# Optimization experiments

Measured on AMD Instinct MI355X. Metric: run time of the kernel, lower is better.

The kernel has to match this reference:

```python
import jax, jax.numpy as jnp
import numpy as np

NY, NX = 2048, 2048
DX = 5.0
DT = 0.8
BETA = 4.0
RHO = 1.0 / 9.81
EPS_ETA = 0.001
MANNING2 = 0.055 ** 2
PAD = ((0, 0), (0, 0), (1, 1), (1, 1))


def _conv3(x, w):
    # 1-channel 3x3 stencil, VALID padding: [1,1,H+2,W+2] -> [1,1,H,W]
    return jax.lax.conv_general_dilated(
        x, w, window_strides=(1, 1), padding='VALID',
        dimension_numbers=('NCHW', 'OIHW', 'NCHW'))


def _bc_u(u):
    # zero left/right columns, copy top/bottom rows (free-slip in y, no-flow in x)
    p = jnp.pad(u, PAD)
    p = p.at[:, :, 0, :].set(p[:, :, 1, :])
    p = p.at[:, :, -1, :].set(p[:, :, -2, :])
    return p


def _bc_v(v):
    # copy left/right columns, zero top/bottom rows
    p = jnp.pad(v, PAD)
    p = p.at[:, :, :, 0].set(p[:, :, :, 1])
    p = p.at[:, :, :, -1].set(p[:, :, :, -2])
    return p


def _bc_eta(h):
    # Neumann (copy) on all four sides; column copies first, then rows (matches torch order)
    p = jnp.pad(h, PAD)
    p = p.at[:, :, :, -1].set(p[:, :, :, -2])
    p = p.at[:, :, :, 0].set(p[:, :, :, 1])
    p = p.at[:, :, -1, :].set(p[:, :, -2, :])
    p = p.at[:, :, 0, :].set(p[:, :, 1, :])
    return p


def _k_pg(wpad, u, v, w1, w2, w3):
    # Petrov-Galerkin dissipation coefficient
    amp = 0.5 * (jnp.abs(u) + jnp.abs(v)) / DX  # = 1/2 dx^-2 (|u|dx + |v|dx)
    num = 0.25 * DX * jnp.abs(amp * _conv3(wpad, w1))
    den = EPS_ETA + 0.5 * (jnp.abs(_conv3(wpad, w2)) + jnp.abs(_conv3(wpad, w3))) / DX ** 2
    return num / den


def _pg_vector(uu, vv, u, v, k3, w1, w2, w3):
    k_u = _k_pg(uu, u, v, w1, w2, w3)
    k_v = _k_pg(vv, u, v, w1, w2, w3)
    k_uu = jnp.pad(jnp.minimum(k_u, k3), PAD)
    k_vv = jnp.pad(jnp.minimum(k_v, k3), PAD)
    k_x = 0.5 * (k_u * _conv3(uu, w1) + _conv3(uu * k_uu, w1) - u * _conv3(k_uu, w1))
    k_y = 0.5 * (k_v * _conv3(vv, w1) + _conv3(vv * k_vv, w1) - v * _conv3(k_vv, w1))
    return k_x, k_y


def _pg_scalar(hh, h, u, v, k3, w1, w2, w3):
    k_u = _k_pg(hh, u, v, w1, w2, w3)
    k_uu = jnp.pad(jnp.minimum(k_u, k3), PAD)
    return 0.5 * (k_u * _conv3(hh, w1) + _conv3(hh * k_uu, w1) - h * _conv3(k_uu, w1))


def _forward(values_u, values_v, values_H, values_h, k1, k2, k3,
             source_h, dif_values_h, values_hh, w1, w2, w3, wm):
    diag = -w1[0, 0, 1, 1]
    uu = _bc_u(values_u)
    vv = _bc_v(values_v)
    k_x, k_y = _pg_vector(uu, vv, values_u, values_v, k3, w1, w2, w3)
    hp = _bc_eta(values_h)
    # predictor (half) step
    b_u = (k_x * DT - values_u * _conv3(uu, w2) * DT - values_v * _conv3(uu, w3) * DT) * 0.5 + values_u
    b_v = (k_y * DT - values_u * _conv3(vv, w2) * DT - values_v * _conv3(vv, w3) * DT) * 0.5 + values_v
    b_u = b_u - _conv3(hp, w2) * DT
    b_v = b_v - _conv3(hp, w3) * DT
    b_uu = _bc_u(b_u)  # note: padded fields built BEFORE friction division, as in source
    b_vv = _bc_v(b_v)
    depth43 = jnp.maximum(k1, values_H + values_h) ** (4.0 / 3.0)
    sigma_q = jnp.sqrt(b_u ** 2 + b_v ** 2) * MANNING2 / depth43
    b_u = b_u / (1.0 + sigma_q * DT / RHO)
    b_v = b_v / (1.0 + sigma_q * DT / RHO)
    # corrector (full) step
    k_x, k_y = _pg_vector(b_uu, b_vv, b_u, b_v, k3, w1, w2, w3)
    u_n = values_u + k_x * DT - b_u * _conv3(b_uu, w2) * DT - b_v * _conv3(b_uu, w3) * DT
    v_n = values_v + k_y * DT - b_u * _conv3(b_vv, w2) * DT - b_v * _conv3(b_vv, w3) * DT
    u_n = u_n - _conv3(hp, w2) * DT
    v_n = v_n - _conv3(hp, w3) * DT
    sigma_q = jnp.sqrt(u_n ** 2 + v_n ** 2) * MANNING2 / depth43
    u_n = u_n / (1.0 + sigma_q * DT / RHO)
    v_n = v_n / (1.0 + sigma_q * DT / RHO)
    uu = _bc_u(u_n)
    vv = _bc_v(v_n)
    eta1 = jnp.maximum(k2, values_H + values_h)
    eta2 = jnp.maximum(k1, values_H + values_h)
    e1p = _bc_eta(eta1)
    b = BETA * RHO * (
        -_conv3(e1p, w2) * u_n - _conv3(e1p, w3) * v_n
        - eta1 * _conv3(uu, w2) - eta1 * _conv3(vv, w3)
        + _pg_scalar(e1p, eta1, u_n, v_n, k3, w1, w2, w3)
        - _conv3(_bc_eta(dif_values_h), wm) / DT
        + source_h) / (DT * eta2)
    # two Jacobi iterations for the wave (pressure) equation
    coef = BETA * RHO / (DT ** 2 * eta2)
    denom = diag + coef
    hh = values_hh
    for _ in range(2):
        hh = hh - (-_conv3(_bc_eta(hh), w1) + coef * hh) / denom + b / denom
    h_new = values_h + hh
    dif_h = h_new - values_h
    hhp = _bc_eta(hh)
    u_n = u_n - _conv3(hhp, w2) * DT / RHO
    v_n = v_n - _conv3(hhp, w3) * DT / RHO
    return (u_n, v_n, h_new, hh, b, dif_h)


def setup_inputs() -> dict:
    key = jax.random.key(0)
    k = jax.random.split(key, 6)
    shape = (1, 1, NY, NX)
    w1 = jnp.asarray(np.array([[1, 1, 1], [1, -8, 1], [1, 1, 1]], np.float32) / 3.0 / DX ** 2).reshape(1, 1, 3, 3)
    w2 = jnp.asarray(np.array([[-1, 0, 1], [-4, 0, 4], [-1, 0, 1]], np.float32) / 12.0 / DX).reshape(1, 1, 3, 3)
    w3 = jnp.transpose(w2, (0, 1, 3, 2))
    wm = jnp.asarray(np.array([[1, 4, 1], [4, 16, 4], [1, 4, 1]], np.float32) / 36.0).reshape(1, 1, 3, 3)
    return {
        'values_u': jax.random.normal(k[0], shape, jnp.float32) * 0.5,
        'values_v': jax.random.normal(k[1], shape, jnp.float32) * 0.5,
        'values_H': jax.random.uniform(k[2], shape, jnp.float32) * 10.0,  # bathymetric depth
        'values_h': jax.random.normal(k[3], shape, jnp.float32) * 0.1,   # free-surface elevation
        'k1': jnp.full(shape, EPS_ETA, jnp.float32),
        'k2': jnp.zeros(shape, jnp.float32),
        'k3': jnp.full(shape, DX ** 2 * 0.1 / DT, jnp.float32),
        'source_h': jax.random.normal(k[4], shape, jnp.float32) * 0.01,
        'dif_values_h': jax.random.normal(k[5], shape, jnp.float32) * 0.01,
        'values_hh': jnp.zeros(shape, jnp.float32),
        'w1': w1, 'w2': w2, 'w3': w3, 'wm': wm,
    }


def reference(values_u, values_v, values_H, values_h, k1, k2, k3,
              source_h, dif_values_h, values_hh, w1, w2, w3, wm):
    return _forward(values_u, values_v, values_H, values_h, k1, k2, k3,
                    source_h, dif_values_h, values_hh, w1, w2, w3, wm)
```

## Files before the change

kernel.cpp:

```cpp
#include <hip/hip_runtime.h>
#include <math.h>


#define NY 2048
#define NX 2048
#define BX 64
#define BY 8
#define GX (NX / BX)
#define GY (NY / BY)
#define KH (BY + 2)
#define KW (BX + 2)
#define TH (BY + 4)
#define TW (BX + 4)

#define DXf   5.0f
#define DTf   0.8f
#define EPSf  0.001f
#define K3f   3.125f

__device__ constexpr float M2f    = (float)(0.055 * 0.055);
__device__ constexpr float RHO_   = (float)(1.0 / 9.81);
__device__ constexpr float BRf    = (float)(4.0 / 9.81);
__device__ constexpr float DT2f   = (float)(0.8 * 0.8);
__device__ constexpr float C43f   = (float)(4.0 / 3.0);
__device__ constexpr float DTRHO  = 0.8f / RHO_;
__device__ constexpr float INVDT  = 1.0f / 0.8f;
__device__ constexpr float CBRDT2 = BRf / DT2f;

#define W1E ((1.0f / 3.0f) / 25.0f)
#define W1C ((-8.0f / 3.0f) / 25.0f)
#define DIAGf ((8.0f / 3.0f) / 25.0f)
#define W2A ((1.0f / 12.0f) / 5.0f)
#define W2B ((4.0f / 12.0f) / 5.0f)
#define WMA (1.0f / 36.0f)
#define WMB (4.0f / 36.0f)
#define WMC (16.0f / 36.0f)

__device__ __forceinline__ int iclamp(int v, int lo, int hi) {
    return v < lo ? lo : (v > hi ? hi : v);
}

__device__ __forceinline__ float frcp(float x) {
    float r = __builtin_amdgcn_rcpf(x);
    return r * (2.0f - x * r);
}

struct N9 { float m[9]; };

template<bool SAFE, int BC>
__device__ __forceinline__ float ld(const float* __restrict__ p, int y, int x) {
    if constexpr (SAFE) {
        if constexpr (BC == 0) {
            if ((unsigned)x >= (unsigned)NX) return 0.0f;
            y = iclamp(y, 0, NY - 1);
        } else if constexpr (BC == 1) {
            if ((unsigned)y >= (unsigned)NY) return 0.0f;
            x = iclamp(x, 0, NX - 1);
        } else {
            y = iclamp(y, 0, NY - 1);
            x = iclamp(x, 0, NX - 1);
        }
    }
    return p[y * NX + x];
}

template<bool SAFE, int BC>
__device__ __forceinline__ N9 ld9(const float* __restrict__ p, int y, int x) {
    N9 n;
#pragma unroll
    for (int dy = 0; dy < 3; ++dy)
#pragma unroll
        for (int dx = 0; dx < 3; ++dx)
            n.m[dy * 3 + dx] = ld<SAFE, BC>(p, y + dy - 1, x + dx - 1);
    return n;
}

template<int W>
__device__ __forceinline__ N9 lds9(const float a[][W], int r, int c) {
    N9 n;
#pragma unroll
    for (int dy = 0; dy < 3; ++dy)
#pragma unroll
        for (int dx = 0; dx < 3; ++dx)
            n.m[dy * 3 + dx] = a[r + dy][c + dx];
    return n;
}

__device__ __forceinline__ float conv1(const N9& n) {
    float nb = n.m[0] + n.m[1] + n.m[2] + n.m[3] + n.m[5] + n.m[6] + n.m[7] + n.m[8];
    return W1E * nb + W1C * n.m[4];
}
__device__ __forceinline__ float conv2(const N9& n) {
    return W2A * ((n.m[2] - n.m[0]) + (n.m[8] - n.m[6])) + W2B * (n.m[5] - n.m[3]);
}
__device__ __forceinline__ float conv3(const N9& n) {
    return W2A * ((n.m[6] - n.m[0]) + (n.m[8] - n.m[2])) + W2B * (n.m[7] - n.m[1]);
}

__device__ __forceinline__ float kpgf(float uq, float vq, float c1, float c2, float c3) {
    float amp = 0.5f * (fabsf(uq) + fabsf(vq)) * 0.2f;
    float num = 1.25f * fabsf(amp * c1);
    float den = EPSf + 0.5f * (fabsf(c2) + fabsf(c3)) * 0.04f;
    return num * frcp(den);
}

__device__ __forceinline__ void prodk(const N9& f, const N9& k, float& pw, float& kw) {
    float nbk = k.m[0] + k.m[1] + k.m[2] + k.m[3] + k.m[5] + k.m[6] + k.m[7] + k.m[8];
    float nbp = f.m[0] * k.m[0] + f.m[1] * k.m[1] + f.m[2] * k.m[2] + f.m[3] * k.m[3]
              + f.m[5] * k.m[5] + f.m[6] * k.m[6] + f.m[7] * k.m[7] + f.m[8] * k.m[8];
    kw = W1E * nbk + W1C * k.m[4];
    pw = W1E * nbp + W1C * (f.m[4] * k.m[4]);
}

template<bool SAFE>
__device__ __forceinline__ void kA_body(
    const float* __restrict__ u, const float* __restrict__ v,
    const float* __restrict__ H, const float* __restrict__ h,
    float* __restrict__ bupre, float* __restrict__ bvpre,
    float* __restrict__ buo, float* __restrict__ bvo,
    float (*skum)[KW], float (*skvm)[KW])
{
    const int tx0 = blockIdx.x * BX, ty0 = blockIdx.y * BY;
    const int lx = threadIdx.x, ly = threadIdx.y;

    for (int r = ly; r < KH; r += BY) {
        int gy = ty0 + r - 1;
        for (int c = lx; c < KW; c += BX) {
            int gx = tx0 + c - 1;
            float kum = 0.f, kvm = 0.f;
            if (!SAFE || ((unsigned)gy < (unsigned)NY && (unsigned)gx < (unsigned)NX)) {
                N9 fu = ld9<SAFE, 0>(u, gy, gx);
                N9 fv = ld9<SAFE, 1>(v, gy, gx);
                float uq = fu.m[4], vq = fv.m[4];
                float ku = kpgf(uq, vq, conv1(fu), conv2(fu), conv3(fu));
                float kv = kpgf(uq, vq, conv1(fv), conv2(fv), conv3(fv));
                kum = fminf(ku, K3f);
                kvm = fminf(kv, K3f);
            }
            skum[r][c] = kum;
            skvm[r][c] = kvm;
        }
    }
    __syncthreads();

    const int y = ty0 + ly, x = tx0 + lx, idx = y * NX + x;
    N9 fu = ld9<SAFE, 0>(u, y, x);
    N9 fv = ld9<SAFE, 1>(v, y, x);
    N9 fh = ld9<SAFE, 2>(h, y, x);
    float uc = fu.m[4], vc = fv.m[4];
    float c1u = conv1(fu), c2u = conv2(fu), c3u = conv3(fu);
    float c1v = conv1(fv), c2v = conv2(fv), c3v = conv3(fv);
    float sku = kpgf(uc, vc, c1u, c2u, c3u);
    float skv = kpgf(uc, vc, c1v, c2v, c3v);

    N9 k9u = lds9<KW>(skum, ly, lx);
    N9 k9v = lds9<KW>(skvm, ly, lx);
    float pwu, kwu, pwv, kwv;
    prodk(fu, k9u, pwu, kwu);
    prodk(fv, k9v, pwv, kwv);
    float kx = 0.5f * (sku * c1u + pwu - uc * kwu);
    float ky = 0.5f * (skv * c1v + pwv - vc * kwv);

    float bu = (kx * DTf - uc * c2u * DTf - vc * c3u * DTf) * 0.5f + uc;
    bu = bu - conv2(fh) * DTf;
    float bv = (ky * DTf - uc * c2v * DTf - vc * c3v * DTf) * 0.5f + vc;
    bv = bv - conv3(fh) * DTf;

    float dep = fmaxf(EPSf, H[idx] + fh.m[4]);
    float d43 = __builtin_amdgcn_exp2f(C43f * __builtin_amdgcn_logf(dep));
    float sq = __builtin_amdgcn_sqrtf(bu * bu + bv * bv) * M2f * frcp(d43);
    float rf = frcp(1.0f + sq * DTRHO);

    bupre[idx] = bu;
    bvpre[idx] = bv;
    buo[idx] = bu * rf;
    bvo[idx] = bv * rf;
}

__global__ __launch_bounds__(512)
void kA(const float* __restrict__ u, const float* __restrict__ v,
        const float* __restrict__ H, const float* __restrict__ h,
        float* __restrict__ bupre, float* __restrict__ bvpre,
        float* __restrict__ buo, float* __restrict__ bvo)
{
    __shared__ float skum[KH][KW], skvm[KH][KW];
    const bool safe = blockIdx.x == 0 || blockIdx.x == GX - 1 ||
                      blockIdx.y == 0 || blockIdx.y == GY - 1;
    if (safe) kA_body<true >(u, v, H, h, bupre, bvpre, buo, bvo, skum, skvm);
    else      kA_body<false>(u, v, H, h, bupre, bvpre, buo, bvo, skum, skvm);
}

template<bool SAFE>
__device__ __forceinline__ void kB_body(
    const float* __restrict__ u, const float* __restrict__ v,
    const float* __restrict__ h, const float* __restrict__ H,
    const float* __restrict__ bupre, const float* __restrict__ bvpre,
    const float* __restrict__ bupost, const float* __restrict__ bvpost,
    float* __restrict__ uno, float* __restrict__ vno,
    float (*skum)[KW], float (*skvm)[KW])
{
    const int tx0 = blockIdx.x * BX, ty0 = blockIdx.y * BY;
    const int lx = threadIdx.x, ly = threadIdx.y;

    for (int r = ly; r < KH; r += BY) {
        int gy = ty0 + r - 1;
        for (int c = lx; c < KW; c += BX) {
            int gx = tx0 + c - 1;
            float kum = 0.f, kvm = 0.f;
            if (!SAFE || ((unsigned)gy < (unsigned)NY && (unsigned)gx < (unsigned)NX)) {
                N9 fu = ld9<SAFE, 0>(bupre, gy, gx);
                N9 fv = ld9<SAFE, 1>(bvpre, gy, gx);
                int gi = gy * NX + gx;
                float uq = bupost[gi], vq = bvpost[gi];
                float ku = kpgf(uq, vq, conv1(fu), conv2(fu), conv3(fu));
                float kv = kpgf(uq, vq, conv1(fv), conv2(fv), conv3(fv));
                kum = fminf(ku, K3f);
                kvm = fminf(kv, K3f);
            }
            skum[r][c] = kum;
            skvm[r][c] = kvm;
        }
    }
    __syncthreads();

    const int y = ty0 + ly, x = tx0 + lx, idx = y * NX + x;
    N9 fu = ld9<SAFE, 0>(bupre, y, x);
    N9 fv = ld9<SAFE, 1>(bvpre, y, x);
    N9 fh = ld9<SAFE, 2>(h, y, x);
    float buc = bupost[idx], bvc = bvpost[idx];
    float c1u = conv1(fu), c2u = conv2(fu), c3u = conv3(fu);
    float c1v = conv1(fv), c2v = conv2(fv), c3v = conv3(fv);
    float sku = kpgf(buc, bvc, c1u, c2u, c3u);
    float skv = kpgf(buc, bvc, c1v, c2v, c3v);

    N9 k9u = lds9<KW>(skum, ly, lx);
    N9 k9v = lds9<KW>(skvm, ly, lx);
    float pwu, kwu, pwv, kwv;
    prodk(fu, k9u, pwu, kwu);
    prodk(fv, k9v, pwv, kwv);
    float kx = 0.5f * (sku * c1u + pwu - buc * kwu);
    float ky = 0.5f * (skv * c1v + pwv - bvc * kwv);

    float un = u[idx] + kx * DTf - buc * c2u * DTf - bvc * c3u * DTf;
    un = un - conv2(fh) * DTf;
    float vn = v[idx] + ky * DTf - buc * c2v * DTf - bvc * c3v * DTf;
    vn = vn - conv3(fh) * DTf;

    float dep = fmaxf(EPSf, H[idx] + fh.m[4]);
    float d43 = __builtin_amdgcn_exp2f(C43f * __builtin_amdgcn_logf(dep));
    float sq = __builtin_amdgcn_sqrtf(un * un + vn * vn) * M2f * frcp(d43);
    float rf = frcp(1.0f + sq * DTRHO);
    uno[idx] = un * rf;
    vno[idx] = vn * rf;
}

__global__ __launch_bounds__(512)
void kB(const float* __restrict__ u, const float* __restrict__ v,
        const float* __restrict__ h, const float* __restrict__ H,
        const float* __restrict__ bupre, const float* __restrict__ bvpre,
        const float* __restrict__ bupost, const float* __restrict__ bvpost,
        float* __restrict__ uno, float* __restrict__ vno)
{
    __shared__ float skum[KH][KW], skvm[KH][KW];
    const bool safe = blockIdx.x == 0 || blockIdx.x == GX - 1 ||
                      blockIdx.y == 0 || blockIdx.y == GY - 1;
    if (safe) kB_body<true >(u, v, h, H, bupre, bvpre, bupost, bvpost, uno, vno, skum, skvm);
    else      kB_body<false>(u, v, h, H, bupre, bvpre, bupost, bvpost, uno, vno, skum, skvm);
}

template<bool SAFE>
__device__ __forceinline__ void kC_body(
    const float* __restrict__ H, const float* __restrict__ h,
    const float* __restrict__ un, const float* __restrict__ vn,
    const float* __restrict__ dif, const float* __restrict__ src,
    const float* __restrict__ hh0,
    float* __restrict__ bo, float* __restrict__ hh1o,
    float (*se)[TW], float (*sksm)[KW])
{
    const int tx0 = blockIdx.x * BX, ty0 = blockIdx.y * BY;
    const int lx = threadIdx.x, ly = threadIdx.y;

    for (int r = ly; r < TH; r += BY) {
        int cy = ty0 + r - 2;
        if (SAFE) cy = iclamp(cy, 0, NY - 1);
        for (int c = lx; c < TW; c += BX) {
            int cx = tx0 + c - 2;
            if (SAFE) cx = iclamp(cx, 0, NX - 1);
            int gi = cy * NX + cx;
            se[r][c] = fmaxf(0.0f, H[gi] + h[gi]);
        }
    }
    __syncthreads();

    for (int r = ly; r < KH; r += BY) {
        int gy = ty0 + r - 1;
        for (int c = lx; c < KW; c += BX) {
            int gx = tx0 + c - 1;
            float ksm = 0.f;
            if (!SAFE || ((unsigned)gy < (unsigned)NY && (unsigned)gx < (unsigned)NX)) {
                N9 fe = lds9<TW>(se, r, c);
                int gi = gy * NX + gx;
                float ks = kpgf(un[gi], vn[gi], conv1(fe), conv2(fe), conv3(fe));
                ksm = fminf(ks, K3f);
            }
            sksm[r][c] = ksm;
        }
    }
    __syncthreads();

    const int y = ty0 + ly, x = tx0 + lx, idx = y * NX + x;
    N9 fe = lds9<TW>(se, ly + 1, lx + 1);
    float e1c = fe.m[4];
    float c1e = conv1(fe), c2e = conv2(fe), c3e = conv3(fe);

    N9 fun = ld9<SAFE, 0>(un, y, x);
    N9 fvn = ld9<SAFE, 1>(vn, y, x);
    float unc = fun.m[4], vnc = fvn.m[4];
    float sks = kpgf(unc, vnc, c1e, c2e, c3e);

    N9 k9 = lds9<KW>(sksm, ly, lx);
    float pw, kw;
    prodk(fe, k9, pw, kw);
    float pg = 0.5f * (sks * c1e + pw - e1c * kw);

    float cw2un = conv2(fun);
    float cw3vn = conv3(fvn);
    N9 fd = ld9<SAFE, 2>(dif, y, x);
    float cwm = WMA * (fd.m[0] + fd.m[2] + fd.m[6] + fd.m[8])
              + WMB * (fd.m[1] + fd.m[3] + fd.m[5] + fd.m[7])
              + WMC * fd.m[4];

    float eta2 = fmaxf(EPSf, e1c);
    float sum = -c2e * unc - c3e * vnc - e1c * cw2un - e1c * cw3vn + pg
              - cwm * INVDT + src[idx];
    float re2 = frcp(eta2);
    float b = (BRf * sum) * INVDT * re2;
    float coef = CBRDT2 * re2;
    float rdn = frcp(DIAGf + coef);

    N9 f0 = ld9<SAFE, 2>(hh0, y, x);
    float hc = f0.m[4];
    float cv = conv1(f0);
    float hh1 = hc + (cv - coef * hc) * rdn + b * rdn;

    bo[idx] = b;
    hh1o[idx] = hh1;
}

__global__ __launch_bounds__(512)
void kC(const float* __restrict__ H, const float* __restrict__ h,
        const float* __restrict__ un, const float* __restrict__ vn,
        const float* __restrict__ dif, const float* __restrict__ src,
        const float* __restrict__ hh0,
        float* __restrict__ bo, float* __restrict__ hh1o)
{
    __shared__ float se[TH][TW];
    __shared__ float sksm[KH][KW];
    const bool safe = blockIdx.x == 0 || blockIdx.x == GX - 1 ||
                      blockIdx.y == 0 || blockIdx.y == GY - 1;
    if (safe) kC_body<true >(H, h, un, vn, dif, src, hh0, bo, hh1o, se, sksm);
    else      kC_body<false>(H, h, un, vn, dif, src, hh0, bo, hh1o, se, sksm);
}

template<bool SAFE>
__device__ __forceinline__ void kD_body(
    const float* __restrict__ H, const float* __restrict__ h,
    const float* __restrict__ un, const float* __restrict__ vn,
    const float* __restrict__ b, const float* __restrict__ hh1,
    float* __restrict__ o_u, float* __restrict__ o_v, float* __restrict__ o_h,
    float* __restrict__ o_hh, float* __restrict__ o_dif,
    float (*s2)[KW])
{
    const int tx0 = blockIdx.x * BX, ty0 = blockIdx.y * BY;
    const int lx = threadIdx.x, ly = threadIdx.y;

    for (int r = ly; r < KH; r += BY) {
        int cy = ty0 + r - 1;
        if (SAFE) cy = iclamp(cy, 0, NY - 1);
        for (int c = lx; c < KW; c += BX) {
            int cx = tx0 + c - 1;
            if (SAFE) cx = iclamp(cx, 0, NX - 1);
            N9 f1 = ld9<SAFE, 2>(hh1, cy, cx);
            float hc = f1.m[4];
            float cv = conv1(f1);
            int gi = cy * NX + cx;
            float coef = CBRDT2 * frcp(fmaxf(EPSf, H[gi] + h[gi]));
            float rdn = frcp(DIAGf + coef);
            s2[r][c] = hc + (cv - coef * hc) * rdn + b[gi] * rdn;
        }
    }
    __syncthreads();

    const int y = ty0 + ly, x = tx0 + lx, idx = y * NX + x;
    N9 p2 = lds9<KW>(s2, ly, lx);
    float hh2 = p2.m[4];
    float hcen = h[idx];
    float hnew = hcen + hh2;

    o_u[idx] = un[idx] - conv2(p2) * DTRHO;
    o_v[idx] = vn[idx] - conv3(p2) * DTRHO;
    o_h[idx] = hnew;
    o_hh[idx] = hh2;
    o_dif[idx] = hnew - hcen;
}

__global__ __launch_bounds__(512)
void kD(const float* __restrict__ H, const float* __restrict__ h,
        const float* __restrict__ un, const float* __restrict__ vn,
        const float* __restrict__ b, const float* __restrict__ hh1,
        float* __restrict__ o_u, float* __restrict__ o_v, float* __restrict__ o_h,
        float* __restrict__ o_hh, float* __restrict__ o_dif)
{
    __shared__ float s2[KH][KW];
    const bool safe = blockIdx.x == 0 || blockIdx.x == GX - 1 ||
                      blockIdx.y == 0 || blockIdx.y == GY - 1;
    if (safe) kD_body<true >(H, h, un, vn, b, hh1, o_u, o_v, o_h, o_hh, o_dif, s2);
    else      kD_body<false>(H, h, un, vn, b, hh1, o_u, o_v, o_h, o_hh, o_dif, s2);
}

extern "C" void kernel_launch(void* const* d_in, const int* in_sizes, int n_in,
                              void* d_out, int out_size, void* d_ws, size_t ws_size,
                              hipStream_t stream)
{
    const float* u   = (const float*)d_in[0];
    const float* v   = (const float*)d_in[1];
    const float* H   = (const float*)d_in[2];
    const float* h   = (const float*)d_in[3];
    const float* src = (const float*)d_in[7];
    const float* dif = (const float*)d_in[8];
    const float* hh0 = (const float*)d_in[9];

    float* out = (float*)d_out;
    const size_t N = (size_t)NY * NX;
    float* o0 = out;
    float* o1 = out + N;
    float* o2 = out + 2 * N;
    float* o3 = out + 3 * N;
    float* o4 = out + 4 * N;
    float* o5 = out + 5 * N;

    float* ws  = (float*)d_ws;
    float* un  = ws;
    float* vn  = ws + N;
    float* hh1 = ws + 2 * N;

    dim3 blk(BX, BY);
    dim3 grd(GX, GY);

    kA<<<grd, blk, 0, stream>>>(u, v, H, h, o0, o1, o3, o4);
    kB<<<grd, blk, 0, stream>>>(u, v, h, H, o0, o1, o3, o4, un, vn);
    kC<<<grd, blk, 0, stream>>>(H, h, un, vn, dif, src, hh0, o4, hh1);
    kD<<<grd, blk, 0, stream>>>(H, h, un, vn, o4, hh1, o0, o1, o2, o3, o5);
}
```

Baseline: 435.5 us.

## Rewrite momentum kernels as register-blocked row-marching stencils without shared memory

kA and kB now have each thread march down eight rows of one column. Stencil rows and the clipped PG coefficient rows stay in rotating registers, so the shared-memory halo, the barrier and the recomputation of k for halo cells are gone. Separable partial sums (A/B/C column combos) cut the arithmetic per stencil. The costs are higher register pressure, fewer threads in flight, and column-neighbour loads that go through L1/L2 instead of LDS. Boundary conditions are handled with clamped indices and multiplicative masks.

```diff
diff --git a/kernel.cpp b/kernel.cpp
--- a/kernel.cpp
+++ b/kernel.cpp
@@ -4,6 +4,8 @@
 
 #define NY 2048
 #define NX 2048
+#define ROWS 8
+
 #define BX 64
 #define BY 8
 #define GX (NX / BX)
@@ -39,13 +41,293 @@
 __device__ __forceinline__ int iclamp(int v, int lo, int hi) {
     return v < lo ? lo : (v > hi ? hi : v);
 }
-
 __device__ __forceinline__ float frcp(float x) {
     float r = __builtin_amdgcn_rcpf(x);
     return r * (2.0f - x * r);
 }
-
-struct N9 { float m[9]; };
+__device__ __forceinline__ float kpgf(float uq, float vq, float c1, float c2, float c3) {
+    float amp = 0.5f * (fabsf(uq) + fabsf(vq)) * 0.2f;
+    float num = 1.25f * fabsf(amp * c1);
+    float den = EPSf + 0.5f * (fabsf(c2) + fabsf(c3)) * 0.04f;
+    return num * frcp(den);
+}
+
+__device__ __forceinline__ void k_row(
+    const float* u0r, const float* u1r, const float* u2r,
+    const float* v0r, const float* v1r, const float* v2r,
+    const float* ampU, const float* ampV,
+    float rowSc, const float* kColS,
+    float* kur, float* kvr, bool save, float* sv)
+{
+    float Au[5], Bu[5], Cu[5], Av[5], Bv[5], Cv[5];
+#pragma unroll
+    for (int c = 0; c < 5; ++c) {
+        Au[c] = (u0r[c] + u1r[c]) + u2r[c];
+        Bu[c] = u2r[c] - u0r[c];
+        Cu[c] = W2A * (u0r[c] + u2r[c]) + W2B * u1r[c];
+        Av[c] = (v0r[c] + v1r[c]) + v2r[c];
+        Bv[c] = v2r[c] - v0r[c];
+        Cv[c] = W2A * (v0r[c] + v2r[c]) + W2B * v1r[c];
+    }
+#pragma unroll
+    for (int j = 0; j < 3; ++j) {
+        const int m = j + 1;
+        float c1u = W1E * ((Au[m-1] + Au[m+1]) + (Au[m] - u1r[m])) + W1C * u1r[m];
+        float c2u = Cu[m+1] - Cu[m-1];
+        float c3u = W2A * (Bu[m-1] + Bu[m+1]) + W2B * Bu[m];
+        float c1v = W1E * ((Av[m-1] + Av[m+1]) + (Av[m] - v1r[m])) + W1C * v1r[m];
+        float c2v = Cv[m+1] - Cv[m-1];
+        float c3v = W2A * (Bv[m-1] + Bv[m+1]) + W2B * Bv[m];
+        float uq = ampU[j], vq = ampV[j];
+        float ku = kpgf(uq, vq, c1u, c2u, c3u);
+        float kv = kpgf(uq, vq, c1v, c2v, c3v);
+        float s = rowSc * kColS[j];
+        kur[j] = fminf(ku, K3f) * s;
+        kvr[j] = fminf(kv, K3f) * s;
+        if (save && j == 1) {
+            sv[0] = c1u; sv[1] = c2u; sv[2] = c3u;
+            sv[3] = c1v; sv[4] = c2v; sv[5] = c3v;
+            sv[6] = ku;  sv[7] = kv;
+        }
+    }
+}
+
+__global__ __launch_bounds__(256)
+void kA(const float* __restrict__ u, const float* __restrict__ v,
+        const float* __restrict__ H, const float* __restrict__ h,
+        float* __restrict__ bupre, float* __restrict__ bvpre,
+        float* __restrict__ buo, float* __restrict__ bvo)
+{
+    const int x  = blockIdx.x * 64 + threadIdx.x;
+    const int y0 = (blockIdx.y * 4 + threadIdx.y) * ROWS;
+
+    int cuI[5]; float cuS[5]; int ceI[5];
+#pragma unroll
+    for (int c = 0; c < 5; ++c) {
+        int cx = x + c - 2;
+        cuI[c] = iclamp(cx, 0, NX - 1);
+        cuS[c] = (cx >= 0 && cx < NX) ? 1.0f : 0.0f;
+        ceI[c] = cuI[c];
+    }
+    float kColS[3] = { x >= 1 ? 1.f : 0.f, 1.f, x <= NX - 2 ? 1.f : 0.f };
+
+    auto loadU = [&](int ry, float* d) {
+        const float* p = u + iclamp(ry, 0, NY - 1) * NX;
+#pragma unroll
+        for (int c = 0; c < 5; ++c) d[c] = p[cuI[c]] * cuS[c];
+    };
+    auto loadV = [&](int ry, float* d) {
+        float s = (ry >= 0 && ry < NY) ? 1.f : 0.f;
+        const float* p = v + iclamp(ry, 0, NY - 1) * NX;
+#pragma unroll
+        for (int c = 0; c < 5; ++c) d[c] = p[ceI[c]] * s;
+    };
+    auto loadH = [&](int ry, float* d) {
+        const float* p = h + iclamp(ry, 0, NY - 1) * NX;
+#pragma unroll
+        for (int c = 0; c < 3; ++c) d[c] = p[ceI[c + 1]];
+    };
+
+    float uA[5], uB[5], u0[5], u1[5], vA[5], vB[5], v0[5], v1[5];
+    loadU(y0 - 2, uA); loadU(y0 - 1, uB); loadU(y0, u0); loadU(y0 + 1, u1);
+    loadV(y0 - 2, vA); loadV(y0 - 1, vB); loadV(y0, v0); loadV(y0 + 1, v1);
+    float hm1[3], h0[3];
+    loadH(y0 - 1, hm1); loadH(y0, h0);
+
+    float kUa[3], kVa[3], kUb[3], kVb[3];
+    float svd[8], sv[8];
+    k_row(uA, uB, u0, vA, vB, v0, &uB[1], &vB[1],
+          (y0 - 1 >= 0) ? 1.f : 0.f, kColS, kUa, kVa, false, svd);
+    k_row(uB, u0, u1, vB, v0, v1, &u0[1], &v0[1],
+          1.f, kColS, kUb, kVb, true, sv);
+    float um1[3] = { uB[1], uB[2], uB[3] }, vm1[3] = { vB[1], vB[2], vB[3] };
+
+#pragma unroll
+    for (int i = 0; i < ROWS; ++i) {
+        const int y = y0 + i;
+        const int idx = y * NX + x;
+        float u2r[5], v2r[5], hL[3];
+        loadU(y + 2, u2r); loadV(y + 2, v2r); loadH(y + 1, hL);
+        float Hc = H[idx];
+
+        float kUc[3], kVc[3], nsv[8];
+        k_row(u0, u1, u2r, v0, v1, v2r, &u1[1], &v1[1],
+              (y + 1 < NY) ? 1.f : 0.f, kColS, kUc, kVc, true, nsv);
+
+        float uc = u0[2], vc = v0[2];
+        float nbku = kUa[0]+kUa[1]+kUa[2] + kUb[0]+kUb[2] + kUc[0]+kUc[1]+kUc[2];
+        float nbpu = um1[0]*kUa[0] + um1[1]*kUa[1] + um1[2]*kUa[2]
+                   + u0[1]*kUb[0] + u0[3]*kUb[2]
+                   + u1[1]*kUc[0] + u1[2]*kUc[1] + u1[3]*kUc[2];
+        float kwu = W1E*nbku + W1C*kUb[1];
+        float pwu = W1E*nbpu + W1C*(uc*kUb[1]);
+        float nbkv = kVa[0]+kVa[1]+kVa[2] + kVb[0]+kVb[2] + kVc[0]+kVc[1]+kVc[2];
+        float nbpv = vm1[0]*kVa[0] + vm1[1]*kVa[1] + vm1[2]*kVa[2]
+                   + v0[1]*kVb[0] + v0[3]*kVb[2]
+                   + v1[1]*kVc[0] + v1[2]*kVc[1] + v1[3]*kVc[2];
+        float kwv = W1E*nbkv + W1C*kVb[1];
+        float pwv = W1E*nbpv + W1C*(vc*kVb[1]);
+
+        float kx = 0.5f * (sv[6]*sv[0] + pwu - uc*kwu);
+        float ky = 0.5f * (sv[7]*sv[3] + pwv - vc*kwv);
+
+        float cw2h = W2A*((hm1[2]-hm1[0]) + (hL[2]-hL[0])) + W2B*(h0[2]-h0[0]);
+        float cw3h = W2A*((hL[0]-hm1[0]) + (hL[2]-hm1[2])) + W2B*(hL[1]-hm1[1]);
+
+        float bu = (kx*DTf - uc*sv[1]*DTf - vc*sv[2]*DTf) * 0.5f + uc;
+        bu = bu - cw2h*DTf;
+        float bv = (ky*DTf - uc*sv[4]*DTf - vc*sv[5]*DTf) * 0.5f + vc;
+        bv = bv - cw3h*DTf;
+
+        float dep = fmaxf(EPSf, Hc + h0[1]);
+        float d43 = __builtin_amdgcn_exp2f(C43f * __builtin_amdgcn_logf(dep));
+        float sq = __builtin_amdgcn_sqrtf(bu*bu + bv*bv) * M2f * frcp(d43);
+        float rf = frcp(1.0f + sq * DTRHO);
+
+        bupre[idx] = bu;
+        bvpre[idx] = bv;
+        buo[idx] = bu * rf;
+        bvo[idx] = bv * rf;
+
+#pragma unroll
+        for (int c = 0; c < 3; ++c) {
+            um1[c] = u0[c+1]; vm1[c] = v0[c+1];
+            hm1[c] = h0[c];   h0[c]  = hL[c];
+            kUa[c] = kUb[c];  kUb[c] = kUc[c];
+            kVa[c] = kVb[c];  kVb[c] = kVc[c];
+        }
+#pragma unroll
+        for (int c = 0; c < 5; ++c) {
+            u0[c] = u1[c]; u1[c] = u2r[c];
+            v0[c] = v1[c]; v1[c] = v2r[c];
+        }
+#pragma unroll
+        for (int c = 0; c < 8; ++c) sv[c] = nsv[c];
+    }
+}
+
+__global__ __launch_bounds__(256)
+void kB(const float* __restrict__ u, const float* __restrict__ v,
+        const float* __restrict__ h, const float* __restrict__ H,
+        const float* __restrict__ bupre, const float* __restrict__ bvpre,
+        const float* __restrict__ bupost, const float* __restrict__ bvpost,
+        float* __restrict__ uno, float* __restrict__ vno)
+{
+    const int x  = blockIdx.x * 64 + threadIdx.x;
+    const int y0 = (blockIdx.y * 4 + threadIdx.y) * ROWS;
+
+    int cuI[5]; float cuS[5]; int ceI[5];
+#pragma unroll
+    for (int c = 0; c < 5; ++c) {
+        int cx = x + c - 2;
+        cuI[c] = iclamp(cx, 0, NX - 1);
+        cuS[c] = (cx >= 0 && cx < NX) ? 1.0f : 0.0f;
+        ceI[c] = cuI[c];
+    }
+    float kColS[3] = { x >= 1 ? 1.f : 0.f, 1.f, x <= NX - 2 ? 1.f : 0.f };
+
+    auto loadBU = [&](int ry, float* d) {
+        const float* p = bupre + iclamp(ry, 0, NY - 1) * NX;
+#pragma unroll
+        for (int c = 0; c < 5; ++c) d[c] = p[cuI[c]] * cuS[c];
+    };
+    auto loadBV = [&](int ry, float* d) {
+        float s = (ry >= 0 && ry < NY) ? 1.f : 0.f;
+        const float* p = bvpre + iclamp(ry, 0, NY - 1) * NX;
+#pragma unroll
+        for (int c = 0; c < 5; ++c) d[c] = p[ceI[c]] * s;
+    };
+    auto loadH = [&](int ry, float* d) {
+        const float* p = h + iclamp(ry, 0, NY - 1) * NX;
+#pragma unroll
+        for (int c = 0; c < 3; ++c) d[c] = p[ceI[c + 1]];
+    };
+    auto loadP = [&](const float* __restrict__ p, int ry, float* d) {
+        const float* q = p + iclamp(ry, 0, NY - 1) * NX;
+#pragma unroll
+        for (int c = 0; c < 3; ++c) d[c] = q[ceI[c + 1]];
+    };
+
+    float uA[5], uB[5], u0[5], u1[5], vA[5], vB[5], v0[5], v1[5];
+    loadBU(y0 - 2, uA); loadBU(y0 - 1, uB); loadBU(y0, u0); loadBU(y0 + 1, u1);
+    loadBV(y0 - 2, vA); loadBV(y0 - 1, vB); loadBV(y0, v0); loadBV(y0 + 1, v1);
+    float hm1[3], h0[3];
+    loadH(y0 - 1, hm1); loadH(y0, h0);
+    float bpA[3], bvA_[3], bpB[3], bvB_[3];
+    loadP(bupost, y0 - 1, bpA); loadP(bvpost, y0 - 1, bvA_);
+    loadP(bupost, y0,     bpB); loadP(bvpost, y0,     bvB_);
+
+    float kUa[3], kVa[3], kUb[3], kVb[3];
+    float svd[8], sv[8];
+    k_row(uA, uB, u0, vA, vB, v0, bpA, bvA_,
+          (y0 - 1 >= 0) ? 1.f : 0.f, kColS, kUa, kVa, false, svd);
+    k_row(uB, u0, u1, vB, v0, v1, bpB, bvB_,
+          1.f, kColS, kUb, kVb, true, sv);
+    float um1[3] = { uB[1], uB[2], uB[3] }, vm1[3] = { vB[1], vB[2], vB[3] };
+    float bpc = bpB[1], bvc = bvB_[1];
+
+#pragma unroll
+    for (int i = 0; i < ROWS; ++i) {
+        const int y = y0 + i;
+        const int idx = y * NX + x;
+        float u2r[5], v2r[5], hL[3], bp1[3], bv1[3];
+        loadBU(y + 2, u2r); loadBV(y + 2, v2r); loadH(y + 1, hL);
+        loadP(bupost, y + 1, bp1); loadP(bvpost, y + 1, bv1);
+
+        float kUc[3], kVc[3], nsv[8];
+        k_row(u0, u1, u2r, v0, v1, v2r, bp1, bv1,
+              (y + 1 < NY) ? 1.f : 0.f, kColS, kUc, kVc, true, nsv);
+
+        float fc_u = u0[2], fc_v = v0[2];
+        float nbku = kUa[0]+kUa[1]+kUa[2] + kUb[0]+kUb[2] + kUc[0]+kUc[1]+kUc[2];
+        float nbpu = um1[0]*kUa[0] + um1[1]*kUa[1] + um1[2]*kUa[2]
+                   + u0[1]*kUb[0] + u0[3]*kUb[2]
+                   + u1[1]*kUc[0] + u1[2]*kUc[1] + u1[3]*kUc[2];
+        float kwu = W1E*nbku + W1C*kUb[1];
+        float pwu = W1E*nbpu + W1C*(fc_u*kUb[1]);
+        float nbkv = kVa[0]+kVa[1]+kVa[2] + kVb[0]+kVb[2] + kVc[0]+kVc[1]+kVc[2];
+        float nbpv = vm1[0]*kVa[0] + vm1[1]*kVa[1] + vm1[2]*kVa[2]
+                   + v0[1]*kVb[0] + v0[3]*kVb[2]
+                   + v1[1]*kVc[0] + v1[2]*kVc[1] + v1[3]*kVc[2];
+        float kwv = W1E*nbkv + W1C*kVb[1];
+        float pwv = W1E*nbpv + W1C*(fc_v*kVb[1]);
+
+        float kx = 0.5f * (sv[6]*sv[0] + pwu - bpc*kwu);
+        float ky = 0.5f * (sv[7]*sv[3] + pwv - bvc*kwv);
+
+        float cw2h = W2A*((hm1[2]-hm1[0]) + (hL[2]-hL[0])) + W2B*(h0[2]-h0[0]);
+        float cw3h = W2A*((hL[0]-hm1[0]) + (hL[2]-hm1[2])) + W2B*(hL[1]-hm1[1]);
+
+        float un = u[idx] + kx*DTf - bpc*sv[1]*DTf - bvc*sv[2]*DTf;
+        un = un - cw2h*DTf;
+        float vn = v[idx] + ky*DTf - bpc*sv[4]*DTf - bvc*sv[5]*DTf;
+        vn = vn - cw3h*DTf;
+
+        float dep = fmaxf(EPSf, H[idx] + h0[1]);
+        float d43 = __builtin_amdgcn_exp2f(C43f * __builtin_amdgcn_logf(dep));
+        float sq = __builtin_amdgcn_sqrtf(un*un + vn*vn) * M2f * frcp(d43);
+        float rf = frcp(1.0f + sq * DTRHO);
+        uno[idx] = un * rf;
+        vno[idx] = vn * rf;
+
+        bpc = bp1[1]; bvc = bv1[1];
+#pragma unroll
+        for (int c = 0; c < 3; ++c) {
+            um1[c] = u0[c+1]; vm1[c] = v0[c+1];
+            hm1[c] = h0[c];   h0[c]  = hL[c];
+            kUa[c] = kUb[c];  kUb[c] = kUc[c];
+            kVa[c] = kVb[c];  kVb[c] = kVc[c];
+        }
+#pragma unroll
+        for (int c = 0; c < 5; ++c) {
+            u0[c] = u1[c]; u1[c] = u2r[c];
+            v0[c] = v1[c]; v1[c] = v2r[c];
+        }
+#pragma unroll
+        for (int c = 0; c < 8; ++c) sv[c] = nsv[c];
+    }
+}
+
 
 template<bool SAFE, int BC>
 __device__ __forceinline__ float ld(const float* __restrict__ p, int y, int x) {
@@ -64,6 +346,8 @@
     return p[y * NX + x];
 }
 
+struct N9 { float m[9]; };
+
 template<bool SAFE, int BC>
 __device__ __forceinline__ N9 ld9(const float* __restrict__ p, int y, int x) {
     N9 n;
@@ -96,176 +380,12 @@
 __device__ __forceinline__ float conv3(const N9& n) {
     return W2A * ((n.m[6] - n.m[0]) + (n.m[8] - n.m[2])) + W2B * (n.m[7] - n.m[1]);
 }
-
-__device__ __forceinline__ float kpgf(float uq, float vq, float c1, float c2, float c3) {
-    float amp = 0.5f * (fabsf(uq) + fabsf(vq)) * 0.2f;
-    float num = 1.25f * fabsf(amp * c1);
-    float den = EPSf + 0.5f * (fabsf(c2) + fabsf(c3)) * 0.04f;
-    return num * frcp(den);
-}
-
 __device__ __forceinline__ void prodk(const N9& f, const N9& k, float& pw, float& kw) {
     float nbk = k.m[0] + k.m[1] + k.m[2] + k.m[3] + k.m[5] + k.m[6] + k.m[7] + k.m[8];
     float nbp = f.m[0] * k.m[0] + f.m[1] * k.m[1] + f.m[2] * k.m[2] + f.m[3] * k.m[3]
               + f.m[5] * k.m[5] + f.m[6] * k.m[6] + f.m[7] * k.m[7] + f.m[8] * k.m[8];
     kw = W1E * nbk + W1C * k.m[4];
     pw = W1E * nbp + W1C * (f.m[4] * k.m[4]);
-}
-
-template<bool SAFE>
-__device__ __forceinline__ void kA_body(
-    const float* __restrict__ u, const float* __restrict__ v,
-    const float* __restrict__ H, const float* __restrict__ h,
-    float* __restrict__ bupre, float* __restrict__ bvpre,
-    float* __restrict__ buo, float* __restrict__ bvo,
-    float (*skum)[KW], float (*skvm)[KW])
-{
-    const int tx0 = blockIdx.x * BX, ty0 = blockIdx.y * BY;
-    const int lx = threadIdx.x, ly = threadIdx.y;
-
-    for (int r = ly; r < KH; r += BY) {
-        int gy = ty0 + r - 1;
-        for (int c = lx; c < KW; c += BX) {
-            int gx = tx0 + c - 1;
-            float kum = 0.f, kvm = 0.f;
-            if (!SAFE || ((unsigned)gy < (unsigned)NY && (unsigned)gx < (unsigned)NX)) {
-                N9 fu = ld9<SAFE, 0>(u, gy, gx);
-                N9 fv = ld9<SAFE, 1>(v, gy, gx);
-                float uq = fu.m[4], vq = fv.m[4];
-                float ku = kpgf(uq, vq, conv1(fu), conv2(fu), conv3(fu));
-                float kv = kpgf(uq, vq, conv1(fv), conv2(fv), conv3(fv));
-                kum = fminf(ku, K3f);
-                kvm = fminf(kv, K3f);
-            }
-            skum[r][c] = kum;
-            skvm[r][c] = kvm;
-        }
-    }
-    __syncthreads();
-
-    const int y = ty0 + ly, x = tx0 + lx, idx = y * NX + x;
-    N9 fu = ld9<SAFE, 0>(u, y, x);
-    N9 fv = ld9<SAFE, 1>(v, y, x);
-    N9 fh = ld9<SAFE, 2>(h, y, x);
-    float uc = fu.m[4], vc = fv.m[4];
-    float c1u = conv1(fu), c2u = conv2(fu), c3u = conv3(fu);
-    float c1v = conv1(fv), c2v = conv2(fv), c3v = conv3(fv);
-    float sku = kpgf(uc, vc, c1u, c2u, c3u);
-    float skv = kpgf(uc, vc, c1v, c2v, c3v);
-
-    N9 k9u = lds9<KW>(skum, ly, lx);
-    N9 k9v = lds9<KW>(skvm, ly, lx);
-    float pwu, kwu, pwv, kwv;
-    prodk(fu, k9u, pwu, kwu);
-    prodk(fv, k9v, pwv, kwv);
-    float kx = 0.5f * (sku * c1u + pwu - uc * kwu);
-    float ky = 0.5f * (skv * c1v + pwv - vc * kwv);
-
-    float bu = (kx * DTf - uc * c2u * DTf - vc * c3u * DTf) * 0.5f + uc;
-    bu = bu - conv2(fh) * DTf;
-    float bv = (ky * DTf - uc * c2v * DTf - vc * c3v * DTf) * 0.5f + vc;
-    bv = bv - conv3(fh) * DTf;
-
-    float dep = fmaxf(EPSf, H[idx] + fh.m[4]);
-    float d43 = __builtin_amdgcn_exp2f(C43f * __builtin_amdgcn_logf(dep));
-    float sq = __builtin_amdgcn_sqrtf(bu * bu + bv * bv) * M2f * frcp(d43);
-    float rf = frcp(1.0f + sq * DTRHO);
-
-    bupre[idx] = bu;
-    bvpre[idx] = bv;
-    buo[idx] = bu * rf;
-    bvo[idx] = bv * rf;
-}
-
-__global__ __launch_bounds__(512)
-void kA(const float* __restrict__ u, const float* __restrict__ v,
-        const float* __restrict__ H, const float* __restrict__ h,
-        float* __restrict__ bupre, float* __restrict__ bvpre,
-        float* __restrict__ buo, float* __restrict__ bvo)
-{
-    __shared__ float skum[KH][KW], skvm[KH][KW];
-    const bool safe = blockIdx.x == 0 || blockIdx.x == GX - 1 ||
-                      blockIdx.y == 0 || blockIdx.y == GY - 1;
-    if (safe) kA_body<true >(u, v, H, h, bupre, bvpre, buo, bvo, skum, skvm);
-    else      kA_body<false>(u, v, H, h, bupre, bvpre, buo, bvo, skum, skvm);
-}
-
-template<bool SAFE>
-__device__ __forceinline__ void kB_body(
-    const float* __restrict__ u, const float* __restrict__ v,
-    const float* __restrict__ h, const float* __restrict__ H,
-    const float* __restrict__ bupre, const float* __restrict__ bvpre,
-    const float* __restrict__ bupost, const float* __restrict__ bvpost,
-    float* __restrict__ uno, float* __restrict__ vno,
-    float (*skum)[KW], float (*skvm)[KW])
-{
-    const int tx0 = blockIdx.x * BX, ty0 = blockIdx.y * BY;
-    const int lx = threadIdx.x, ly = threadIdx.y;
-
-    for (int r = ly; r < KH; r += BY) {
-        int gy = ty0 + r - 1;
-        for (int c = lx; c < KW; c += BX) {
-            int gx = tx0 + c - 1;
-            float kum = 0.f, kvm = 0.f;
-            if (!SAFE || ((unsigned)gy < (unsigned)NY && (unsigned)gx < (unsigned)NX)) {
-                N9 fu = ld9<SAFE, 0>(bupre, gy, gx);
-                N9 fv = ld9<SAFE, 1>(bvpre, gy, gx);
-                int gi = gy * NX + gx;
-                float uq = bupost[gi], vq = bvpost[gi];
-                float ku = kpgf(uq, vq, conv1(fu), conv2(fu), conv3(fu));
-                float kv = kpgf(uq, vq, conv1(fv), conv2(fv), conv3(fv));
-                kum = fminf(ku, K3f);
-                kvm = fminf(kv, K3f);
-            }
-            skum[r][c] = kum;
-            skvm[r][c] = kvm;
-        }
-    }
-    __syncthreads();
-
-    const int y = ty0 + ly, x = tx0 + lx, idx = y * NX + x;
-    N9 fu = ld9<SAFE, 0>(bupre, y, x);
-    N9 fv = ld9<SAFE, 1>(bvpre, y, x);
-    N9 fh = ld9<SAFE, 2>(h, y, x);
-    float buc = bupost[idx], bvc = bvpost[idx];
-    float c1u = conv1(fu), c2u = conv2(fu), c3u = conv3(fu);
-    float c1v = conv1(fv), c2v = conv2(fv), c3v = conv3(fv);
-    float sku = kpgf(buc, bvc, c1u, c2u, c3u);
-    float skv = kpgf(buc, bvc, c1v, c2v, c3v);
-
-    N9 k9u = lds9<KW>(skum, ly, lx);
-    N9 k9v = lds9<KW>(skvm, ly, lx);
-    float pwu, kwu, pwv, kwv;
-    prodk(fu, k9u, pwu, kwu);
-    prodk(fv, k9v, pwv, kwv);
-    float kx = 0.5f * (sku * c1u + pwu - buc * kwu);
-    float ky = 0.5f * (skv * c1v + pwv - bvc * kwv);
-
-    float un = u[idx] + kx * DTf - buc * c2u * DTf - bvc * c3u * DTf;
-    un = un - conv2(fh) * DTf;
-    float vn = v[idx] + ky * DTf - buc * c2v * DTf - bvc * c3v * DTf;
-    vn = vn - conv3(fh) * DTf;
-
-    float dep = fmaxf(EPSf, H[idx] + fh.m[4]);
-    float d43 = __builtin_amdgcn_exp2f(C43f * __builtin_amdgcn_logf(dep));
-    float sq = __builtin_amdgcn_sqrtf(un * un + vn * vn) * M2f * frcp(d43);
-    float rf = frcp(1.0f + sq * DTRHO);
-    uno[idx] = un * rf;
-    vno[idx] = vn * rf;
-}
-
-__global__ __launch_bounds__(512)
-void kB(const float* __restrict__ u, const float* __restrict__ v,
-        const float* __restrict__ h, const float* __restrict__ H,
-        const float* __restrict__ bupre, const float* __restrict__ bvpre,
-        const float* __restrict__ bupost, const float* __restrict__ bvpost,
-        float* __restrict__ uno, float* __restrict__ vno)
-{
-    __shared__ float skum[KH][KW], skvm[KH][KW];
-    const bool safe = blockIdx.x == 0 || blockIdx.x == GX - 1 ||
-                      blockIdx.y == 0 || blockIdx.y == GY - 1;
-    if (safe) kB_body<true >(u, v, h, H, bupre, bvpre, bupost, bvpost, uno, vno, skum, skvm);
-    else      kB_body<false>(u, v, h, H, bupre, bvpre, bupost, bvpost, uno, vno, skum, skvm);
 }
 
 template<bool SAFE>
@@ -444,11 +564,13 @@
     float* vn  = ws + N;
     float* hh1 = ws + 2 * N;
 
-    dim3 blk(BX, BY);
-    dim3 grd(GX, GY);
-
-    kA<<<grd, blk, 0, stream>>>(u, v, H, h, o0, o1, o3, o4);
-    kB<<<grd, blk, 0, stream>>>(u, v, h, H, o0, o1, o3, o4, un, vn);
-    kC<<<grd, blk, 0, stream>>>(H, h, un, vn, dif, src, hh0, o4, hh1);
-    kD<<<grd, blk, 0, stream>>>(H, h, un, vn, o4, hh1, o0, o1, o2, o3, o5);
-}
+    dim3 rblk(64, 4);
+    dim3 rgrd(NX / 64, NY / (4 * ROWS));
+    dim3 tblk(BX, BY);
+    dim3 tgrd(GX, GY);
+
+    kA<<<rgrd, rblk, 0, stream>>>(u, v, H, h, o0, o1, o3, o4);
+    kB<<<rgrd, rblk, 0, stream>>>(u, v, h, H, o0, o1, o3, o4, un, vn);
+    kC<<<tgrd, tblk, 0, stream>>>(H, h, un, vn, dif, src, hh0, o4, hh1);
+    kD<<<tgrd, tblk, 0, stream>>>(H, h, un, vn, o4, hh1, o0, o1, o2, o3, o5);
+}
```

Measured after the change: 394.0 us. 9.5% less time.
